# Kernel tuning notes

Measured on AMD Instinct MI355X. Metric: run time of the kernel, lower is better.

The kernel has to match this reference:

```python
import jax, jax.numpy as jnp
import numpy as np

B, S, H, NH, FF = 16, 1024, 768, 12, 3072
D = H // NH  # 64
EPS = 1e-12


def layer_norm(x, g, b):
    mu = jnp.mean(x, axis=-1, keepdims=True)
    var = jnp.mean(jnp.square(x - mu), axis=-1, keepdims=True)
    return (x - mu) * jax.lax.rsqrt(var + EPS) * g + b


def setup_inputs() -> dict:
    key = jax.random.key(0)
    ks = jax.random.split(key, 16)
    w = lambda k, shape: (jax.random.normal(k, shape, jnp.float32) * 0.02)
    return {
        "features": jax.random.normal(ks[0], (B, S, H), jnp.float32),
        "attention_mask": jnp.zeros((B, S), jnp.float32),  # additive mask
        "wq": w(ks[1], (H, H)), "bq": jnp.zeros((H,), jnp.float32),
        "wk": w(ks[2], (H, H)), "bk": jnp.zeros((H,), jnp.float32),
        "wv": w(ks[3], (H, H)), "bv": jnp.zeros((H,), jnp.float32),
        "wo": w(ks[4], (H, H)), "bo": jnp.zeros((H,), jnp.float32),
        "ln1_g": jnp.ones((H,), jnp.float32), "ln1_b": jnp.zeros((H,), jnp.float32),
        "w1": w(ks[5], (H, FF)), "b1": jnp.zeros((FF,), jnp.float32),
        "w2": w(ks[6], (FF, H)), "b2": jnp.zeros((H,), jnp.float32),
        "ln2_g": jnp.ones((H,), jnp.float32), "ln2_b": jnp.zeros((H,), jnp.float32),
        "wp": w(ks[7], (H, H)), "bp": jnp.zeros((H,), jnp.float32),
        "wm": w(ks[8], (H, 1)), "bm": jnp.zeros((1,), jnp.float32),
    }


def reference(features, attention_mask, wq, bq, wk, bk, wv, bv, wo, bo,
              ln1_g, ln1_b, w1, b1, w2, b2, ln2_g, ln2_b, wp, bp, wm, bm):
    mask = attention_mask[:, None, None, :]  # [B,1,1,S]

    def split_heads(x):  # [B,S,H] -> [B,NH,S,D]
        return x.reshape(B, S, NH, D).transpose(0, 2, 1, 3)

    q = split_heads(features @ wq + bq)
    k = split_heads(features @ wk + bk)
    v = split_heads(features @ wv + bv)

    scores = jnp.einsum("bhqd,bhkd->bhqk", q, k) / np.sqrt(D).astype(np.float32)
    probs = jax.nn.softmax(scores + mask, axis=-1)  # dropout is identity (eval)
    ctx = jnp.einsum("bhqk,bhkd->bhqd", probs, v)
    ctx = ctx.transpose(0, 2, 1, 3).reshape(B, S, H)

    attn_out = layer_norm(ctx @ wo + bo + features, ln1_g, ln1_b)
    ffn = jax.nn.gelu(attn_out @ w1 + b1, approximate=False) @ w2 + b2
    hidden = layer_norm(ffn + attn_out, ln2_g, ln2_b)

    pooled = jnp.tanh(hidden[:, 0] @ wp + bp)  # BertPooler on [CLS]
    cls = (pooled @ wm + bm).squeeze()  # [B]
    return cls
```

## Files before the change

kernel.cpp:

```cpp
#include <hip/hip_runtime.h>
#include <math.h>

namespace {

constexpr int B  = 16;
constexpr int S  = 1024;
constexpr int H  = 768;
constexpr int NH = 12;
constexpr int DH = 64;
constexpr int FF = 3072;
constexpr int KSPL = 8;
constexpr float EPS = 1e-12f;

__device__ __forceinline__ float waveReduceSum(float v) {
#pragma unroll
    for (int d = 1; d < 64; d <<= 1) v += __shfl_xor(v, d);
    return v;
}

__device__ __forceinline__ float blockReduceSum768(float v, float* red) {
    const int lane = threadIdx.x & 63;
    const int wid  = threadIdx.x >> 6;
    v = waveReduceSum(v);
    __syncthreads();
    if (lane == 0) red[wid] = v;
    __syncthreads();
    float s = 0.f;
#pragma unroll
    for (int w = 0; w < 12; ++w) s += red[w];
    return s;
}

template <int K, int ISPL, int N>
__global__ __launch_bounds__(256) void gemm_partial(
        const float* __restrict__ A, int lda, int jtOfsA,
        const float* __restrict__ W, float* __restrict__ part) {
    constexpr int IR = K / ISPL;
    __shared__ float Asl[B * IR];
    const int jt  = blockIdx.x;
    const int sp  = blockIdx.y;
    const int i0  = sp * IR;
    const int tid = threadIdx.x;

    for (int e = tid; e < B * IR; e += 256) {
        const int b = e / IR, ii = e % IR;
        Asl[e] = A[(size_t)b * lda + (size_t)jt * jtOfsA + i0 + ii];
    }
    __syncthreads();

    const int jl = tid & 63;
    const int bg = tid >> 6;
    const int j  = jt * 64 + jl;
    const float* wp_ = W + (size_t)i0 * N + j;
    const float* a0 = Asl + (bg * 4 + 0) * IR;
    const float* a1 = Asl + (bg * 4 + 1) * IR;
    const float* a2 = Asl + (bg * 4 + 2) * IR;
    const float* a3 = Asl + (bg * 4 + 3) * IR;
    float acc0 = 0.f, acc1 = 0.f, acc2 = 0.f, acc3 = 0.f;
#pragma unroll 8
    for (int ii = 0; ii < IR; ++ii) {
        const float w = wp_[(size_t)ii * N];
        acc0 += w * a0[ii];
        acc1 += w * a1[ii];
        acc2 += w * a2[ii];
        acc3 += w * a3[ii];
    }
    float* pp = part + ((size_t)sp * B) * N + j;
    pp[(size_t)(bg * 4 + 0) * N] = acc0;
    pp[(size_t)(bg * 4 + 1) * N] = acc1;
    pp[(size_t)(bg * 4 + 2) * N] = acc2;
    pp[(size_t)(bg * 4 + 3) * N] = acc3;
}

template <int K, int ISPL, int N, int RED>
__global__ __launch_bounds__(256) void gemm_partial_red(
        const float* __restrict__ Ain, const float* __restrict__ bias,
        const float* __restrict__ W, float* __restrict__ part) {
    constexpr int IR = K / ISPL;
    __shared__ float Asl[B * IR];
    const int jt  = blockIdx.x;
    const int sp  = blockIdx.y;
    const int i0  = sp * IR;
    const int tid = threadIdx.x;

    for (int e = tid; e < B * IR; e += 256) {
        const int b = e / IR, ii = e % IR;
        float v = bias[i0 + ii];
#pragma unroll
        for (int sp2 = 0; sp2 < RED; ++sp2)
            v += Ain[((size_t)sp2 * B + b) * K + i0 + ii];
        Asl[e] = v;
    }
    __syncthreads();

    const int jl = tid & 63;
    const int bg = tid >> 6;
    const int j  = jt * 64 + jl;
    const float* wp_ = W + (size_t)i0 * N + j;
    const float* a0 = Asl + (bg * 4 + 0) * IR;
    const float* a1 = Asl + (bg * 4 + 1) * IR;
    const float* a2 = Asl + (bg * 4 + 2) * IR;
    const float* a3 = Asl + (bg * 4 + 3) * IR;
    float acc0 = 0.f, acc1 = 0.f, acc2 = 0.f, acc3 = 0.f;
#pragma unroll 8
    for (int ii = 0; ii < IR; ++ii) {
        const float w = wp_[(size_t)ii * N];
        acc0 += w * a0[ii];
        acc1 += w * a1[ii];
        acc2 += w * a2[ii];
        acc3 += w * a3[ii];
    }
    float* pp = part + ((size_t)sp * B) * N + j;
    pp[(size_t)(bg * 4 + 0) * N] = acc0;
    pp[(size_t)(bg * 4 + 1) * N] = acc1;
    pp[(size_t)(bg * 4 + 2) * N] = acc2;
    pp[(size_t)(bg * 4 + 3) * N] = acc3;
}

template <int ISPL, int N>
__global__ __launch_bounds__(256) void reduce_bias_gelu(
        const float* __restrict__ part, const float* __restrict__ bias,
        float* __restrict__ out) {
    const int e = blockIdx.x * 256 + threadIdx.x;
    if (e >= B * N) return;
    const int b = e / N, j = e % N;
    float s = bias[j];
#pragma unroll
    for (int sp = 0; sp < ISPL; ++sp) s += part[((size_t)sp * B + b) * N + j];
    out[e] = 0.5f * s * (1.0f + erff(s * 0.70710678118654752440f));
}

__global__ __launch_bounds__(256) void u_kernel(
        const float* __restrict__ q0_part, const float* __restrict__ bq,
        const float* __restrict__ wk, const float* __restrict__ bk,
        float* __restrict__ u, float* __restrict__ constk) {
    const int b = blockIdx.x / NH, h = blockIdx.x % NH;
    __shared__ float qh[DH];
    const int tid = threadIdx.x;
    if (tid < DH) {
        float v = bq[h * DH + tid];
#pragma unroll
        for (int sp = 0; sp < 24; ++sp)
            v += q0_part[((size_t)sp * B + b) * H + h * DH + tid];
        qh[tid] = v;
    }
    __syncthreads();
    if (tid < DH) {
        float v = bk[h * DH + tid] * qh[tid];
        v = waveReduceSum(v);
        if (tid == 0) constk[b * NH + h] = v;
    }
    const int jj = tid & 3, iq = tid >> 2;
    const float4* qv = (const float4*)qh;
    float4 q4[4];
#pragma unroll
    for (int c = 0; c < 4; ++c) q4[c] = qv[jj * 4 + c];
#pragma unroll
    for (int ir = 0; ir < 12; ++ir) {
        const int i = ir * 64 + iq;
        const float4* wr = (const float4*)(wk + (size_t)i * H + h * DH);
        float s = 0.f;
#pragma unroll
        for (int c = 0; c < 4; ++c) {
            const float4 w = wr[jj * 4 + c];
            s += w.x * q4[c].x + w.y * q4[c].y + w.z * q4[c].z + w.w * q4[c].w;
        }
        s += __shfl_xor(s, 1);
        s += __shfl_xor(s, 2);
        if (jj == 0) u[((size_t)(b * NH + h)) * H + i] = s;
    }
}

__global__ __launch_bounds__(256, 2) void score_kernel(
        const float* __restrict__ x, const float* __restrict__ u,
        const float* __restrict__ constk, const float* __restrict__ mask,
        float* __restrict__ scores) {
    const int b  = blockIdx.x;
    const int kt = blockIdx.y;
    __shared__ __align__(16) float ul[NH * H];
    __shared__ float ck[NH];
    const int tid = threadIdx.x;
    {
        const float4* ug = (const float4*)(u + (size_t)b * NH * H);
        float4* ul4 = (float4*)ul;
        for (int e = tid; e < NH * H / 4; e += 256) ul4[e] = ug[e];
        if (tid < NH) ck[tid] = constk[b * NH + tid];
    }
    __syncthreads();

    const int jj = tid & 15, kk = tid >> 4;
    const int k0 = kt * 32 + kk * 2;
    float4 xv0[12], xv1[12];
    {
        const float4* xr0 = (const float4*)(x + ((size_t)b * S + k0) * H);
        const float4* xr1 = (const float4*)(x + ((size_t)b * S + k0 + 1) * H);
#pragma unroll
        for (int t = 0; t < 12; ++t) { xv0[t] = xr0[jj + 16 * t]; xv1[t] = xr1[jj + 16 * t]; }
    }
    const float4* ul4 = (const float4*)ul;
    float acc0[NH], acc1[NH];
#pragma unroll
    for (int h = 0; h < NH; ++h) {
        float a0 = 0.f, a1 = 0.f;
#pragma unroll
        for (int t = 0; t < 12; ++t) {
            const float4 uv = ul4[h * 192 + jj + 16 * t];
            a0 += xv0[t].x * uv.x + xv0[t].y * uv.y + xv0[t].z * uv.z + xv0[t].w * uv.w;
            a1 += xv1[t].x * uv.x + xv1[t].y * uv.y + xv1[t].z * uv.z + xv1[t].w * uv.w;
        }
        acc0[h] = a0; acc1[h] = a1;
    }
#pragma unroll
    for (int h = 0; h < NH; ++h) {
#pragma unroll
        for (int d = 1; d < 16; d <<= 1) {
            acc0[h] += __shfl_xor(acc0[h], d);
            acc1[h] += __shfl_xor(acc1[h], d);
        }
    }
    if (jj == 0) {
        const float mk0 = mask[b * S + k0];
        const float mk1 = mask[b * S + k0 + 1];
#pragma unroll
        for (int h = 0; h < NH; ++h) {
            scores[((size_t)(b * NH + h)) * S + k0]     = acc0[h] * 0.125f + ck[h] + mk0;
            scores[((size_t)(b * NH + h)) * S + k0 + 1] = acc1[h] * 0.125f + ck[h] + mk1;
        }
    }
}

__global__ __launch_bounds__(256) void softmax_kernel(
        const float* __restrict__ scores, float* __restrict__ p_t) {
    const int bh = blockIdx.x;
    const int b = bh / NH, h = bh % NH;
    const float* p = scores + (size_t)bh * S;
    const int tid = threadIdx.x, wid = tid >> 6, lane = tid & 63;
    float4 v = *(const float4*)(p + tid * 4);
    __shared__ float redm[4], reds[4];
    float m = fmaxf(fmaxf(v.x, v.y), fmaxf(v.z, v.w));
#pragma unroll
    for (int d = 1; d < 64; d <<= 1) m = fmaxf(m, __shfl_xor(m, d));
    if (lane == 0) redm[wid] = m;
    __syncthreads();
    m = fmaxf(fmaxf(redm[0], redm[1]), fmaxf(redm[2], redm[3]));
    v.x = expf(v.x - m); v.y = expf(v.y - m);
    v.z = expf(v.z - m); v.w = expf(v.w - m);
    float s = v.x + v.y + v.z + v.w;
    s = waveReduceSum(s);
    if (lane == 0) reds[wid] = s;
    __syncthreads();
    s = reds[0] + reds[1] + reds[2] + reds[3];
    const float inv = 1.0f / s;
    float* pt = p_t + ((size_t)b * S + tid * 4) * NH + h;
    pt[0 * NH] = v.x * inv;
    pt[1 * NH] = v.y * inv;
    pt[2 * NH] = v.z * inv;
    pt[3 * NH] = v.w * inv;
}

__global__ __launch_bounds__(768) void xbar_partial(
        const float* __restrict__ x, const float* __restrict__ p_t,
        float* __restrict__ xpart) {
    constexpr int KR = S / KSPL;
    const int b = blockIdx.x, sp = blockIdx.y;
    const int tid = threadIdx.x;
    float acc[NH];
#pragma unroll
    for (int h = 0; h < NH; ++h) acc[h] = 0.f;
    const float* xr = x + ((size_t)b * S + sp * KR) * H + tid;
    const float* pr = p_t + ((size_t)b * S + sp * KR) * NH;
#pragma unroll 4
    for (int kk = 0; kk < KR; ++kk) {
        const float xv = xr[(size_t)kk * H];
#pragma unroll
        for (int h = 0; h < NH; ++h) acc[h] += pr[kk * NH + h] * xv;
    }
    float* op = xpart + ((size_t)(b * KSPL + sp)) * NH * H + tid;
#pragma unroll
    for (int h = 0; h < NH; ++h) op[(size_t)h * H] = acc[h];
}

__global__ __launch_bounds__(256) void xbar_reduce(
        const float* __restrict__ xpart, float* __restrict__ xbar) {
    const int e = blockIdx.x * 256 + threadIdx.x;
    if (e >= B * NH * H) return;
    const int b = e / (NH * H), rem = e % (NH * H);
    float s = 0.f;
#pragma unroll
    for (int sp = 0; sp < KSPL; ++sp)
        s += xpart[((size_t)(b * KSPL + sp)) * NH * H + rem];
    xbar[e] = s;
}

template <int ISPL>
__global__ __launch_bounds__(768) void ln_kernel(
        const float* __restrict__ part, const float* __restrict__ bias,
        const float* __restrict__ resid, int residStride,
        const float* __restrict__ g, const float* __restrict__ bet,
        float* __restrict__ out) {
    __shared__ float red[12];
    const int b = blockIdx.x, j = threadIdx.x;
    float v = bias[j] + resid[(size_t)b * residStride + j];
#pragma unroll
    for (int sp = 0; sp < ISPL; ++sp) v += part[((size_t)sp * B + b) * H + j];
    const float mu = blockReduceSum768(v, red) * (1.0f / H);
    const float d  = v - mu;
    const float var = blockReduceSum768(d * d, red) * (1.0f / H);
    out[(size_t)b * H + j] = d * rsqrtf(var + EPS) * g[j] + bet[j];
}

template <int ISPL>
__global__ __launch_bounds__(768) void cls_kernel(
        const float* __restrict__ part, const float* __restrict__ bp,
        const float* __restrict__ wm, const float* __restrict__ bm,
        float* __restrict__ out) {
    __shared__ float red[12];
    const int b = blockIdx.x, j = threadIdx.x;
    float v = bp[j];
#pragma unroll
    for (int sp = 0; sp < ISPL; ++sp) v += part[((size_t)sp * B + b) * H + j];
    v = tanhf(v);
    const float s = blockReduceSum768(v * wm[j], red);
    if (j == 0) out[b] = s + bm[0];
}

}

extern "C" void kernel_launch(void* const* d_in, const int* in_sizes, int n_in,
                              void* d_out, int out_size, void* d_ws, size_t ws_size,
                              hipStream_t stream) {
    const float* x    = (const float*)d_in[0];
    const float* mask = (const float*)d_in[1];
    const float* wq   = (const float*)d_in[2];
    const float* bq   = (const float*)d_in[3];
    const float* wk   = (const float*)d_in[4];
    const float* bk   = (const float*)d_in[5];
    const float* wv   = (const float*)d_in[6];
    const float* bv   = (const float*)d_in[7];
    const float* wo   = (const float*)d_in[8];
    const float* bo   = (const float*)d_in[9];
    const float* ln1g = (const float*)d_in[10];
    const float* ln1b = (const float*)d_in[11];
    const float* w1   = (const float*)d_in[12];
    const float* b1   = (const float*)d_in[13];
    const float* w2   = (const float*)d_in[14];
    const float* b2   = (const float*)d_in[15];
    const float* ln2g = (const float*)d_in[16];
    const float* ln2b = (const float*)d_in[17];
    const float* wp   = (const float*)d_in[18];
    const float* bp   = (const float*)d_in[19];
    const float* wm   = (const float*)d_in[20];
    const float* bm   = (const float*)d_in[21];
    float* out = (float*)d_out;

    float* ws = (float*)d_ws;
    size_t o = 0;
    float* u        = ws + o; o += (size_t)B * NH * H;
    float* constk   = ws + o; o += 256;
    float* p_t      = ws + o; o += (size_t)B * S * NH;
    float* xbar     = ws + o; o += (size_t)B * NH * H;
    float* attn_out = ws + o; o += (size_t)B * H;
    float* tbuf     = ws + o; o += (size_t)B * FF;
    float* hidden   = ws + o; o += (size_t)B * H;
    float* arena    = ws + o;
    float* q0_part   = arena;
    float* scores    = arena;
    float* xpart     = arena;
    float* ctx_part  = arena;
    float* wo_part   = arena + (size_t)24 * B * H;
    float* ffn1_part = arena;
    float* ffn2_part = arena;
    float* pool_part = arena;
    (void)ws_size; (void)in_sizes; (void)n_in; (void)out_size;

    gemm_partial<H, 24, H><<<dim3(12, 24), 256, 0, stream>>>(x, S * H, 0, wq, q0_part);

    u_kernel<<<B * NH, 256, 0, stream>>>(q0_part, bq, wk, bk, u, constk);

    score_kernel<<<dim3(B, S / 32), 256, 0, stream>>>(x, u, constk, mask, scores);

    softmax_kernel<<<B * NH, 256, 0, stream>>>(scores, p_t);

    xbar_partial<<<dim3(B, KSPL), 768, 0, stream>>>(x, p_t, xpart);
    xbar_reduce<<<(B * NH * H + 255) / 256, 256, 0, stream>>>(xpart, xbar);

    gemm_partial<H, 24, H><<<dim3(12, 24), 256, 0, stream>>>(xbar, NH * H, H, wv, ctx_part);

    gemm_partial_red<H, 24, H, 24><<<dim3(12, 24), 256, 0, stream>>>(ctx_part, bv, wo, wo_part);
    ln_kernel<24><<<B, 768, 0, stream>>>(wo_part, bo, x, S * H, ln1g, ln1b, attn_out);

    gemm_partial<H, 24, FF><<<dim3(48, 24), 256, 0, stream>>>(attn_out, H, 0, w1, ffn1_part);
    reduce_bias_gelu<24, FF><<<192, 256, 0, stream>>>(ffn1_part, b1, tbuf);
    gemm_partial<FF, 48, H><<<dim3(12, 48), 256, 0, stream>>>(tbuf, FF, 0, w2, ffn2_part);
    ln_kernel<48><<<B, 768, 0, stream>>>(ffn2_part, b2, attn_out, H, ln2g, ln2b, hidden);

    gemm_partial<H, 24, H><<<dim3(12, 24), 256, 0, stream>>>(hidden, H, 0, wp, pool_part);
    cls_kernel<24><<<B, 768, 0, stream>>>(pool_part, bp, wm, bm, out);
}
```

Before: 235.6 us.

## Fuse softmax into score kernel and fold reductions into downstream GEMMs

The score kernel now computes exponentials directly and writes per-block partial row sums, so the separate softmax kernel goes away. xbar_partial applies the normalisation from those partial sums. The xbar_reduce pass is folded into a new gemm_xpart that sums the KSPL partials while loading its tile. The bias+GELU reduction is likewise folded into the W2 GEMM prologue. KSPL doubles to 16 and several unroll pragmas change. Dropping the max subtraction in softmax removes a pass and a barrier, but it can overflow if scores are large.

```diff
diff --git a/kernel.cpp b/kernel.cpp
--- a/kernel.cpp
+++ b/kernel.cpp
@@ -9,7 +9,7 @@
 constexpr int NH = 12;
 constexpr int DH = 64;
 constexpr int FF = 3072;
-constexpr int KSPL = 8;
+constexpr int KSPL = 16;
 constexpr float EPS = 1e-12f;
 
 __device__ __forceinline__ float waveReduceSum(float v) {
@@ -57,7 +57,7 @@
     const float* a2 = Asl + (bg * 4 + 2) * IR;
     const float* a3 = Asl + (bg * 4 + 3) * IR;
     float acc0 = 0.f, acc1 = 0.f, acc2 = 0.f, acc3 = 0.f;
-#pragma unroll 8
+#pragma unroll
     for (int ii = 0; ii < IR; ++ii) {
         const float w = wp_[(size_t)ii * N];
         acc0 += w * a0[ii];
@@ -102,7 +102,7 @@
     const float* a2 = Asl + (bg * 4 + 2) * IR;
     const float* a3 = Asl + (bg * 4 + 3) * IR;
     float acc0 = 0.f, acc1 = 0.f, acc2 = 0.f, acc3 = 0.f;
-#pragma unroll 8
+#pragma unroll
     for (int ii = 0; ii < IR; ++ii) {
         const float w = wp_[(size_t)ii * N];
         acc0 += w * a0[ii];
@@ -117,17 +117,94 @@
     pp[(size_t)(bg * 4 + 3) * N] = acc3;
 }
 
-template <int ISPL, int N>
-__global__ __launch_bounds__(256) void reduce_bias_gelu(
-        const float* __restrict__ part, const float* __restrict__ bias,
-        float* __restrict__ out) {
-    const int e = blockIdx.x * 256 + threadIdx.x;
-    if (e >= B * N) return;
-    const int b = e / N, j = e % N;
-    float s = bias[j];
-#pragma unroll
-    for (int sp = 0; sp < ISPL; ++sp) s += part[((size_t)sp * B + b) * N + j];
-    out[e] = 0.5f * s * (1.0f + erff(s * 0.70710678118654752440f));
+template <int K, int ISPL, int N, int RED>
+__global__ __launch_bounds__(256) void gemm_partial_red_gelu(
+        const float* __restrict__ Ain, const float* __restrict__ bias,
+        const float* __restrict__ W, float* __restrict__ part) {
+    constexpr int IR = K / ISPL;
+    __shared__ float Asl[B * IR];
+    const int jt  = blockIdx.x;
+    const int sp  = blockIdx.y;
+    const int i0  = sp * IR;
+    const int tid = threadIdx.x;
+
+    for (int e = tid; e < B * IR; e += 256) {
+        const int b = e / IR, ii = e % IR;
+        float v = bias[i0 + ii];
+#pragma unroll
+        for (int sp2 = 0; sp2 < RED; ++sp2)
+            v += Ain[((size_t)sp2 * B + b) * K + i0 + ii];
+        Asl[e] = 0.5f * v * (1.0f + erff(v * 0.70710678118654752440f));
+    }
+    __syncthreads();
+
+    const int jl = tid & 63;
+    const int bg = tid >> 6;
+    const int j  = jt * 64 + jl;
+    const float* wp_ = W + (size_t)i0 * N + j;
+    const float* a0 = Asl + (bg * 4 + 0) * IR;
+    const float* a1 = Asl + (bg * 4 + 1) * IR;
+    const float* a2 = Asl + (bg * 4 + 2) * IR;
+    const float* a3 = Asl + (bg * 4 + 3) * IR;
+    float acc0 = 0.f, acc1 = 0.f, acc2 = 0.f, acc3 = 0.f;
+#pragma unroll 32
+    for (int ii = 0; ii < IR; ++ii) {
+        const float w = wp_[(size_t)ii * N];
+        acc0 += w * a0[ii];
+        acc1 += w * a1[ii];
+        acc2 += w * a2[ii];
+        acc3 += w * a3[ii];
+    }
+    float* pp = part + ((size_t)sp * B) * N + j;
+    pp[(size_t)(bg * 4 + 0) * N] = acc0;
+    pp[(size_t)(bg * 4 + 1) * N] = acc1;
+    pp[(size_t)(bg * 4 + 2) * N] = acc2;
+    pp[(size_t)(bg * 4 + 3) * N] = acc3;
+}
+
+template <int ISPL>
+__global__ __launch_bounds__(256) void gemm_xpart(
+        const float* __restrict__ xpart, const float* __restrict__ W,
+        float* __restrict__ part) {
+    constexpr int IR = H / ISPL;
+    __shared__ float Asl[B * IR];
+    const int jt  = blockIdx.x;
+    const int sp  = blockIdx.y;
+    const int i0  = sp * IR;
+    const int tid = threadIdx.x;
+
+    for (int e = tid; e < B * IR; e += 256) {
+        const int b = e / IR, ii = e % IR;
+        float v = 0.f;
+#pragma unroll
+        for (int s2 = 0; s2 < KSPL; ++s2)
+            v += xpart[(((size_t)(b * KSPL + s2)) * NH + jt) * H + i0 + ii];
+        Asl[e] = v;
+    }
+    __syncthreads();
+
+    const int jl = tid & 63;
+    const int bg = tid >> 6;
+    const int j  = jt * 64 + jl;
+    const float* wp_ = W + (size_t)i0 * H + j;
+    const float* a0 = Asl + (bg * 4 + 0) * IR;
+    const float* a1 = Asl + (bg * 4 + 1) * IR;
+    const float* a2 = Asl + (bg * 4 + 2) * IR;
+    const float* a3 = Asl + (bg * 4 + 3) * IR;
+    float acc0 = 0.f, acc1 = 0.f, acc2 = 0.f, acc3 = 0.f;
+#pragma unroll
+    for (int ii = 0; ii < IR; ++ii) {
+        const float w = wp_[(size_t)ii * H];
+        acc0 += w * a0[ii];
+        acc1 += w * a1[ii];
+        acc2 += w * a2[ii];
+        acc3 += w * a3[ii];
+    }
+    float* pp = part + ((size_t)sp * B) * H + j;
+    pp[(size_t)(bg * 4 + 0) * H] = acc0;
+    pp[(size_t)(bg * 4 + 1) * H] = acc1;
+    pp[(size_t)(bg * 4 + 2) * H] = acc2;
+    pp[(size_t)(bg * 4 + 3) * H] = acc3;
 }
 
 __global__ __launch_bounds__(256) void u_kernel(
@@ -155,7 +232,7 @@
     float4 q4[4];
 #pragma unroll
     for (int c = 0; c < 4; ++c) q4[c] = qv[jj * 4 + c];
-#pragma unroll
+#pragma unroll 4
     for (int ir = 0; ir < 12; ++ir) {
         const int i = ir * 64 + iq;
         const float4* wr = (const float4*)(wk + (size_t)i * H + h * DH);
@@ -174,11 +251,12 @@
 __global__ __launch_bounds__(256, 2) void score_kernel(
         const float* __restrict__ x, const float* __restrict__ u,
         const float* __restrict__ constk, const float* __restrict__ mask,
-        float* __restrict__ scores) {
+        float* __restrict__ e_t, float* __restrict__ psum) {
     const int b  = blockIdx.x;
     const int kt = blockIdx.y;
     __shared__ __align__(16) float ul[NH * H];
     __shared__ float ck[NH];
+    __shared__ float wsum[4][NH];
     const int tid = threadIdx.x;
     {
         const float4* ug = (const float4*)(u + (size_t)b * NH * H);
@@ -218,78 +296,69 @@
             acc1[h] += __shfl_xor(acc1[h], d);
         }
     }
+    const float mk0 = mask[b * S + k0];
+    const float mk1 = mask[b * S + k0 + 1];
+    float e0[NH], e1[NH], ps[NH];
+#pragma unroll
+    for (int h = 0; h < NH; ++h) {
+        e0[h] = expf(acc0[h] * 0.125f + ck[h] + mk0);
+        e1[h] = expf(acc1[h] * 0.125f + ck[h] + mk1);
+        ps[h] = e0[h] + e1[h];
+    }
     if (jj == 0) {
-        const float mk0 = mask[b * S + k0];
-        const float mk1 = mask[b * S + k0 + 1];
-#pragma unroll
-        for (int h = 0; h < NH; ++h) {
-            scores[((size_t)(b * NH + h)) * S + k0]     = acc0[h] * 0.125f + ck[h] + mk0;
-            scores[((size_t)(b * NH + h)) * S + k0 + 1] = acc1[h] * 0.125f + ck[h] + mk1;
-        }
-    }
-}
-
-__global__ __launch_bounds__(256) void softmax_kernel(
-        const float* __restrict__ scores, float* __restrict__ p_t) {
-    const int bh = blockIdx.x;
-    const int b = bh / NH, h = bh % NH;
-    const float* p = scores + (size_t)bh * S;
-    const int tid = threadIdx.x, wid = tid >> 6, lane = tid & 63;
-    float4 v = *(const float4*)(p + tid * 4);
-    __shared__ float redm[4], reds[4];
-    float m = fmaxf(fmaxf(v.x, v.y), fmaxf(v.z, v.w));
-#pragma unroll
-    for (int d = 1; d < 64; d <<= 1) m = fmaxf(m, __shfl_xor(m, d));
-    if (lane == 0) redm[wid] = m;
-    __syncthreads();
-    m = fmaxf(fmaxf(redm[0], redm[1]), fmaxf(redm[2], redm[3]));
-    v.x = expf(v.x - m); v.y = expf(v.y - m);
-    v.z = expf(v.z - m); v.w = expf(v.w - m);
-    float s = v.x + v.y + v.z + v.w;
-    s = waveReduceSum(s);
-    if (lane == 0) reds[wid] = s;
-    __syncthreads();
-    s = reds[0] + reds[1] + reds[2] + reds[3];
-    const float inv = 1.0f / s;
-    float* pt = p_t + ((size_t)b * S + tid * 4) * NH + h;
-    pt[0 * NH] = v.x * inv;
-    pt[1 * NH] = v.y * inv;
-    pt[2 * NH] = v.z * inv;
-    pt[3 * NH] = v.w * inv;
+        float4* er0 = (float4*)(e_t + ((size_t)(b * S + k0)) * NH);
+        float4* er1 = (float4*)(e_t + ((size_t)(b * S + k0 + 1)) * NH);
+        er0[0] = make_float4(e0[0], e0[1], e0[2], e0[3]);
+        er0[1] = make_float4(e0[4], e0[5], e0[6], e0[7]);
+        er0[2] = make_float4(e0[8], e0[9], e0[10], e0[11]);
+        er1[0] = make_float4(e1[0], e1[1], e1[2], e1[3]);
+        er1[1] = make_float4(e1[4], e1[5], e1[6], e1[7]);
+        er1[2] = make_float4(e1[8], e1[9], e1[10], e1[11]);
+    }
+#pragma unroll
+    for (int h = 0; h < NH; ++h) {
+        ps[h] += __shfl_xor(ps[h], 16);
+        ps[h] += __shfl_xor(ps[h], 32);
+    }
+    const int wid = tid >> 6;
+    if ((tid & 63) == 0) {
+#pragma unroll
+        for (int h = 0; h < NH; ++h) wsum[wid][h] = ps[h];
+    }
+    __syncthreads();
+    if (tid < NH)
+        psum[((size_t)(b * 32 + kt)) * NH + tid] =
+            wsum[0][tid] + wsum[1][tid] + wsum[2][tid] + wsum[3][tid];
 }
 
 __global__ __launch_bounds__(768) void xbar_partial(
-        const float* __restrict__ x, const float* __restrict__ p_t,
-        float* __restrict__ xpart) {
+        const float* __restrict__ x, const float* __restrict__ e_t,
+        const float* __restrict__ psum, float* __restrict__ xpart) {
     constexpr int KR = S / KSPL;
     const int b = blockIdx.x, sp = blockIdx.y;
     const int tid = threadIdx.x;
+    __shared__ float rinv[NH];
+    if (tid < NH) {
+        float s = 0.f;
+#pragma unroll
+        for (int kt = 0; kt < 32; ++kt) s += psum[((size_t)(b * 32 + kt)) * NH + tid];
+        rinv[tid] = 1.0f / s;
+    }
     float acc[NH];
 #pragma unroll
     for (int h = 0; h < NH; ++h) acc[h] = 0.f;
     const float* xr = x + ((size_t)b * S + sp * KR) * H + tid;
-    const float* pr = p_t + ((size_t)b * S + sp * KR) * NH;
-#pragma unroll 4
+    const float* er = e_t + ((size_t)b * S + sp * KR) * NH;
+#pragma unroll 8
     for (int kk = 0; kk < KR; ++kk) {
         const float xv = xr[(size_t)kk * H];
 #pragma unroll
-        for (int h = 0; h < NH; ++h) acc[h] += pr[kk * NH + h] * xv;
-    }
+        for (int h = 0; h < NH; ++h) acc[h] += er[kk * NH + h] * xv;
+    }
+    __syncthreads();
     float* op = xpart + ((size_t)(b * KSPL + sp)) * NH * H + tid;
 #pragma unroll
-    for (int h = 0; h < NH; ++h) op[(size_t)h * H] = acc[h];
-}
-
-__global__ __launch_bounds__(256) void xbar_reduce(
-        const float* __restrict__ xpart, float* __restrict__ xbar) {
-    const int e = blockIdx.x * 256 + threadIdx.x;
-    if (e >= B * NH * H) return;
-    const int b = e / (NH * H), rem = e % (NH * H);
-    float s = 0.f;
-#pragma unroll
-    for (int sp = 0; sp < KSPL; ++sp)
-        s += xpart[((size_t)(b * KSPL + sp)) * NH * H + rem];
-    xbar[e] = s;
+    for (int h = 0; h < NH; ++h) op[(size_t)h * H] = acc[h] * rinv[h];
 }
 
 template <int ISPL>
@@ -357,19 +426,17 @@
     size_t o = 0;
     float* u        = ws + o; o += (size_t)B * NH * H;
     float* constk   = ws + o; o += 256;
-    float* p_t      = ws + o; o += (size_t)B * S * NH;
-    float* xbar     = ws + o; o += (size_t)B * NH * H;
+    float* e_t      = ws + o; o += (size_t)B * S * NH;
+    float* psum     = ws + o; o += (size_t)B * 32 * NH;
     float* attn_out = ws + o; o += (size_t)B * H;
-    float* tbuf     = ws + o; o += (size_t)B * FF;
     float* hidden   = ws + o; o += (size_t)B * H;
     float* arena    = ws + o;
     float* q0_part   = arena;
-    float* scores    = arena;
     float* xpart     = arena;
-    float* ctx_part  = arena;
-    float* wo_part   = arena + (size_t)24 * B * H;
+    float* ctx_part  = arena + (size_t)KSPL * B * NH * H;
+    float* wo_part   = ctx_part + (size_t)24 * B * H;
     float* ffn1_part = arena;
-    float* ffn2_part = arena;
+    float* ffn2_part = arena + (size_t)24 * B * FF;
     float* pool_part = arena;
     (void)ws_size; (void)in_sizes; (void)n_in; (void)out_size;
 
@@ -377,21 +444,17 @@
 
     u_kernel<<<B * NH, 256, 0, stream>>>(q0_part, bq, wk, bk, u, constk);
 
-    score_kernel<<<dim3(B, S / 32), 256, 0, stream>>>(x, u, constk, mask, scores);
-
-    softmax_kernel<<<B * NH, 256, 0, stream>>>(scores, p_t);
-
-    xbar_partial<<<dim3(B, KSPL), 768, 0, stream>>>(x, p_t, xpart);
-    xbar_reduce<<<(B * NH * H + 255) / 256, 256, 0, stream>>>(xpart, xbar);
-
-    gemm_partial<H, 24, H><<<dim3(12, 24), 256, 0, stream>>>(xbar, NH * H, H, wv, ctx_part);
+    score_kernel<<<dim3(B, S / 32), 256, 0, stream>>>(x, u, constk, mask, e_t, psum);
+
+    xbar_partial<<<dim3(B, KSPL), 768, 0, stream>>>(x, e_t, psum, xpart);
+
+    gemm_xpart<24><<<dim3(12, 24), 256, 0, stream>>>(xpart, wv, ctx_part);
 
     gemm_partial_red<H, 24, H, 24><<<dim3(12, 24), 256, 0, stream>>>(ctx_part, bv, wo, wo_part);
     ln_kernel<24><<<B, 768, 0, stream>>>(wo_part, bo, x, S * H, ln1g, ln1b, attn_out);
 
     gemm_partial<H, 24, FF><<<dim3(48, 24), 256, 0, stream>>>(attn_out, H, 0, w1, ffn1_part);
-    reduce_bias_gelu<24, FF><<<192, 256, 0, stream>>>(ffn1_part, b1, tbuf);
-    gemm_partial<FF, 48, H><<<dim3(12, 48), 256, 0, stream>>>(tbuf, FF, 0, w2, ffn2_part);
+    gemm_partial_red_gelu<FF, 48, H, 24><<<dim3(12, 48), 256, 0, stream>>>(ffn1_part, b1, w2, ffn2_part);
     ln_kernel<48><<<B, 768, 0, stream>>>(ffn2_part, b2, attn_out, H, ln2g, ln2b, hidden);
 
     gemm_partial<H, 24, H><<<dim3(12, 24), 256, 0, stream>>>(hidden, H, 0, wp, pool_part);
```

After: 210.6 us. 10.6% less time.
